# Performance work log

Hardware: AMD Instinct MI355X
Metric: run time of the kernel (lower is better)

The kernel has to match this reference:

```python
import jax, jax.numpy as jnp
import numpy as np
import math

N_HEADS = 16
D_MODEL = 1024
DK = D_MODEL // N_HEADS
B, S = 2, 2048


def setup_inputs() -> dict:
    key = jax.random.key(0)
    ks = jax.random.split(key, 11)
    scale_in = 1.0 / math.sqrt(D_MODEL)
    scale_o = 1.0 / math.sqrt(N_HEADS * DK)
    return {
        "query": jax.random.normal(ks[0], (B, S, D_MODEL), jnp.float32),
        "key": jax.random.normal(ks[1], (B, S, D_MODEL), jnp.float32),
        "value": jax.random.normal(ks[2], (B, S, D_MODEL), jnp.float32),
        # stacked per-head projection weights [H, d_model, dk], biases [H, dk]
        "Wq": jax.random.normal(ks[3], (N_HEADS, D_MODEL, DK), jnp.float32) * scale_in,
        "bq": jax.random.normal(ks[4], (N_HEADS, DK), jnp.float32) * scale_in,
        "Wk": jax.random.normal(ks[5], (N_HEADS, D_MODEL, DK), jnp.float32) * scale_in,
        "bk": jax.random.normal(ks[6], (N_HEADS, DK), jnp.float32) * scale_in,
        "Wv": jax.random.normal(ks[7], (N_HEADS, D_MODEL, DK), jnp.float32) * scale_in,
        "bv": jax.random.normal(ks[8], (N_HEADS, DK), jnp.float32) * scale_in,
        "Wo": jax.random.normal(ks[9], (N_HEADS * DK, D_MODEL), jnp.float32) * scale_o,
        "bo": jax.random.normal(ks[10], (D_MODEL,), jnp.float32) * scale_o,
    }


def reference(query, key, value, Wq, bq, Wk, bk, Wv, bv, Wo, bo):
    # Per-head linear projections, vectorized over heads: [B,H,S,dk]
    q = jnp.einsum("bsd,hdk->bhsk", query, Wq) + bq[None, :, None, :]
    k = jnp.einsum("bsd,hdk->bhsk", key, Wk) + bk[None, :, None, :]
    v = jnp.einsum("bsd,hdk->bhsk", value, Wv) + bv[None, :, None, :]
    # Scaled dot-product scores [B,H,S,S]
    scores = jnp.einsum("bhsk,bhtk->bhst", q, k) / jnp.sqrt(jnp.asarray(DK, q.dtype))
    # FAITHFUL to source: nn.Softmax(dim=0) -> softmax over the BATCH axis
    attn = jax.nn.softmax(scores, axis=0)
    out = jnp.einsum("bhst,bhtk->bhsk", attn, v)  # [B,H,S,dk]
    # concat heads along feature dim (torch.cat dim=2)
    concat = out.transpose(0, 2, 1, 3).reshape(query.shape[0], query.shape[1], N_HEADS * DK)
    return concat @ Wo + bo
```

## Files before the change

kernel.cpp:

```cpp
#include <hip/hip_runtime.h>
#include <hip/hip_bf16.h>

#define B_ 2
#define S_ 2048
#define D_ 1024
#define H_ 16
#define DK_ 64
#define BS_ (B_ * S_)

typedef unsigned int u32;
typedef unsigned short u16;
typedef __attribute__((ext_vector_type(8))) short bf16x8;
typedef __attribute__((ext_vector_type(4))) float f32x4;

__device__ __forceinline__ float bf2f(u16 v) {
    union { u32 u; float f; } c; c.u = ((u32)v) << 16; return c.f;
}
__device__ __forceinline__ u16 f2bf(float f) {
    union { float f; u32 u; } c; c.f = f;
    u32 u = c.u;
    return (u16)((u + 0x7fffu + ((u >> 16) & 1u)) >> 16);
}
__device__ __forceinline__ u32 packtr(float lo, float hi) {
    union { float f; u32 u; } a, b; a.f = lo; b.f = hi;
    return __builtin_amdgcn_perm(b.u, a.u, 0x07060302u);
}
__device__ __forceinline__ int sw64(int r, int c8) { return (((c8) + (r)) & 7) * 8; }
__device__ __forceinline__ int sw32(int r, int c8) { return (((c8) + (r)) & 3) * 8; }

struct WArgs { const float* W[4]; u16* WT[4]; };
__global__ __launch_bounds__(256) void prep_w(WArgs wa)
{
    __shared__ __attribute__((aligned(16))) u16 T[64][72];
    const int z = blockIdx.z;
    const float* W = wa.W[z];
    u16* WT = wa.WT[z];
    const int headMode = (z < 3) ? 1 : 0;
    const int tid = threadIdx.x;
    const int k0 = blockIdx.x * 64;
    const int n0 = blockIdx.y * 64;
    const int kr = tid >> 4;
    const int n4 = (tid & 15) * 4;
    #pragma unroll
    for (int pass = 0; pass < 4; ++pass) {
        int kk = k0 + pass * 16 + kr;
        const float* p = headMode
            ? (W + (size_t)((n0 + n4) >> 6) * (1024 * 64) + kk * 64 + ((n0 + n4) & 63))
            : (W + (size_t)kk * 1024 + n0 + n4);
        float4 a = *(const float4*)p;
        int krel = pass * 16 + kr;
        T[n4 + 0][krel] = f2bf(a.x);
        T[n4 + 1][krel] = f2bf(a.y);
        T[n4 + 2][krel] = f2bf(a.z);
        T[n4 + 3][krel] = f2bf(a.w);
    }
    __syncthreads();
    const int nr = tid >> 2;
    const int kq = (tid & 3) * 16;
    uint4 o0 = *(const uint4*)&T[nr][kq];
    uint4 o1 = *(const uint4*)&T[nr][kq + 8];
    u16* q = WT + (size_t)(n0 + nr) * 1024 + k0 + kq;
    *(uint4*)q = o0;
    *(uint4*)(q + 8) = o1;
}

__global__ __launch_bounds__(256) void vprep(
    const u16* __restrict__ Vb, u16* __restrict__ VT, float* __restrict__ csums)
{
    __shared__ __attribute__((aligned(16))) u16 T[64][72];
    __shared__ float red[256];
    const int tid = threadIdx.x;
    const int t0 = blockIdx.x * 64;
    const int bh = blockIdx.y;
    const int b = bh >> 4, h = bh & 15;
    const int tr = tid >> 4;
    const int d4 = (tid & 15) * 4;
    #pragma unroll
    for (int pass = 0; pass < 4; ++pass) {
        int tt = t0 + pass * 16 + tr;
        const u16* p = Vb + (size_t)(b * S_ + tt) * 1024 + h * 64 + d4;
        u32 a = *(const u32*)p;
        u32 c = *(const u32*)(p + 2);
        int trel = pass * 16 + tr;
        T[d4 + 0][trel] = (u16)a;
        T[d4 + 1][trel] = (u16)(a >> 16);
        T[d4 + 2][trel] = (u16)c;
        T[d4 + 3][trel] = (u16)(c >> 16);
    }
    __syncthreads();
    const int dr = tid >> 2;
    const int tq = (tid & 3) * 16;
    uint4 o0 = *(const uint4*)&T[dr][tq];
    uint4 o1 = *(const uint4*)&T[dr][tq + 8];
    u16* q = VT + ((size_t)bh * 64 + dr) * 2048 + t0 + tq;
    *(uint4*)q = o0;
    *(uint4*)(q + 8) = o1;

    if (b == 1) {
        const int dk = tid & 63, part = tid >> 6;
        float s = 0.f;
        #pragma unroll
        for (int t = 0; t < 16; ++t) s += bf2f(T[dk][part * 16 + t]);
        red[tid] = s;
        __syncthreads();
        if (tid < 64)
            atomicAdd(&csums[h * 64 + tid],
                      red[tid] + red[tid + 64] + red[tid + 128] + red[tid + 192]);
    }
}

struct ProjArgs {
    const float* X[3];
    const u16* W[3];
    const float* bias[3];
    u16* Y[3];
};
__global__ __launch_bounds__(256) void proj3(ProjArgs pa)
{
    __shared__ __attribute__((aligned(16))) u16 As[128][32];
    __shared__ __attribute__((aligned(16))) u16 Bs[64][32];
    const int z = blockIdx.z;
    const float* X = pa.X[z];
    const u16* WT = pa.W[z];
    const float* bias = pa.bias[z];
    u16* Y = pa.Y[z];
    const int neg = (z == 1);

    const int tid = threadIdx.x;
    const int lane = tid & 63;
    const int wave = tid >> 6;
    const int quad = lane >> 4;
    const int l16 = lane & 15;
    const int m0 = blockIdx.x * 128;
    const int n0 = blockIdx.y * 64;
    const int wm = (wave & 1) * 64, wn = (wave >> 1) * 32;

    const int srow = tid >> 1, half = tid & 1;
    const int brow = tid >> 2, bc8 = tid & 3;

    f32x4 acc[4][2] = {};

    for (int k0 = 0; k0 < 1024; k0 += 32) {
        __syncthreads();
        {
            const float* p = X + (size_t)(m0 + srow) * 1024 + k0 + half * 16;
            float4 a0 = *(const float4*)(p + 0);
            float4 a1 = *(const float4*)(p + 4);
            float4 a2 = *(const float4*)(p + 8);
            float4 a3 = *(const float4*)(p + 12);
            uint4 w0 = make_uint4(packtr(a0.x, a0.y), packtr(a0.z, a0.w),
                                  packtr(a1.x, a1.y), packtr(a1.z, a1.w));
            uint4 w1 = make_uint4(packtr(a2.x, a2.y), packtr(a2.z, a2.w),
                                  packtr(a3.x, a3.y), packtr(a3.z, a3.w));
            const int c8 = half * 2;
            *(uint4*)&As[srow][sw32(srow, c8)]     = w0;
            *(uint4*)&As[srow][sw32(srow, c8 + 1)] = w1;
            *(uint4*)&Bs[brow][sw32(brow, bc8)] =
                *(const uint4*)(WT + (size_t)(n0 + brow) * 1024 + k0 + bc8 * 8);
        }
        __syncthreads();
        bf16x8 af[4], bfr[2];
        #pragma unroll
        for (int mt = 0; mt < 4; ++mt) {
            const int r = wm + mt * 16 + l16;
            af[mt] = *(const bf16x8*)&As[r][sw32(r, quad)];
        }
        #pragma unroll
        for (int nt = 0; nt < 2; ++nt) {
            const int r = wn + nt * 16 + l16;
            bfr[nt] = *(const bf16x8*)&Bs[r][sw32(r, quad)];
        }
        #pragma unroll
        for (int mt = 0; mt < 4; ++mt)
            #pragma unroll
            for (int nt = 0; nt < 2; ++nt)
                acc[mt][nt] = __builtin_amdgcn_mfma_f32_16x16x32_bf16(
                    af[mt], bfr[nt], acc[mt][nt], 0, 0, 0);
    }

    #pragma unroll
    for (int nt = 0; nt < 2; ++nt) {
        const int col = n0 + wn + nt * 16 + l16;
        const float bv = bias[col];
        #pragma unroll
        for (int mt = 0; mt < 4; ++mt) {
            #pragma unroll
            for (int r = 0; r < 4; ++r) {
                const int row = m0 + wm + mt * 16 + quad * 4 + r;
                float v = acc[mt][nt][r] + bv;
                if (neg && row >= 2048) v = -v;
                Y[(size_t)row * 1024 + col] = f2bf(v);
            }
        }
    }
}

__global__ __launch_bounds__(256) void gemm_out(
    const u16* __restrict__ X, const u16* __restrict__ WT,
    const float* __restrict__ bias, float* __restrict__ Y)
{
    __shared__ __attribute__((aligned(16))) u16 As[128][32];
    __shared__ __attribute__((aligned(16))) u16 Bs[64][32];
    const int tid = threadIdx.x;
    const int lane = tid & 63;
    const int wave = tid >> 6;
    const int quad = lane >> 4;
    const int l16 = lane & 15;
    const int m0 = blockIdx.x * 128;
    const int n0 = blockIdx.y * 64;
    const int wm = (wave & 1) * 64, wn = (wave >> 1) * 32;

    const int srow = tid >> 1, half = tid & 1;
    const int brow = tid >> 2, bc8 = tid & 3;

    f32x4 acc[4][2] = {};

    for (int k0 = 0; k0 < 1024; k0 += 32) {
        __syncthreads();
        {
            const u16* p = X + (size_t)(m0 + srow) * 1024 + k0 + half * 16;
            const int c8 = half * 2;
            *(uint4*)&As[srow][sw32(srow, c8)]     = *(const uint4*)p;
            *(uint4*)&As[srow][sw32(srow, c8 + 1)] = *(const uint4*)(p + 8);
            *(uint4*)&Bs[brow][sw32(brow, bc8)] =
                *(const uint4*)(WT + (size_t)(n0 + brow) * 1024 + k0 + bc8 * 8);
        }
        __syncthreads();
        bf16x8 af[4], bfr[2];
        #pragma unroll
        for (int mt = 0; mt < 4; ++mt) {
            const int r = wm + mt * 16 + l16;
            af[mt] = *(const bf16x8*)&As[r][sw32(r, quad)];
        }
        #pragma unroll
        for (int nt = 0; nt < 2; ++nt) {
            const int r = wn + nt * 16 + l16;
            bfr[nt] = *(const bf16x8*)&Bs[r][sw32(r, quad)];
        }
        #pragma unroll
        for (int mt = 0; mt < 4; ++mt)
            #pragma unroll
            for (int nt = 0; nt < 2; ++nt)
                acc[mt][nt] = __builtin_amdgcn_mfma_f32_16x16x32_bf16(
                    af[mt], bfr[nt], acc[mt][nt], 0, 0, 0);
    }

    #pragma unroll
    for (int nt = 0; nt < 2; ++nt) {
        const int col = n0 + wn + nt * 16 + l16;
        const float bv = bias[col];
        #pragma unroll
        for (int mt = 0; mt < 4; ++mt) {
            #pragma unroll
            for (int r = 0; r < 4; ++r) {
                const int row = m0 + wm + mt * 16 + quad * 4 + r;
                Y[(size_t)row * 1024 + col] = acc[mt][nt][r] + bv;
            }
        }
    }
}

__global__ __launch_bounds__(256) void attn_mfma(
    const u16* __restrict__ Qb, const u16* __restrict__ Kb,
    const u16* __restrict__ VT, const float* __restrict__ csums,
    u16* __restrict__ Cc)
{
    __shared__ __attribute__((aligned(16))) u16 Ks[2][64][64];
    __shared__ __attribute__((aligned(16))) u16 Vs[2][64][64];
    __shared__ __attribute__((aligned(16))) u16 Ps[64][64];

    const int id = blockIdx.x;
    const int xcd = id & 7, j = id >> 3;
    const int h = xcd + 8 * (j >> 5);
    const int s0 = (j & 31) * 64;

    const int tid = threadIdx.x;
    const int lane = tid & 63;
    const int wave = tid >> 6;
    const int quad = lane >> 4;
    const int l16 = lane & 15;
    const int sw = wave * 16;

    const int r_ = tid >> 2;
    const int cq = (tid & 3) * 16;
    const int cq8 = (tid & 3) * 2;

    bf16x8 qf[2][2];
    #pragma unroll
    for (int b = 0; b < 2; ++b)
        #pragma unroll
        for (int ks = 0; ks < 2; ++ks)
            qf[b][ks] = *(const bf16x8*)(Qb + (size_t)(b * S_ + s0 + sw + l16) * 1024
                                          + h * 64 + ks * 32 + quad * 8);

    f32x4 O0[4] = {}, T1[4] = {};

    for (int t0 = 0; t0 < S_; t0 += 64) {
        __syncthreads();
        #pragma unroll
        for (int b = 0; b < 2; ++b) {
            const u16* pk = Kb + (size_t)(b * S_ + t0 + r_) * 1024 + h * 64 + cq;
            *(uint4*)&Ks[b][r_][sw64(r_, cq8)]     = *(const uint4*)pk;
            *(uint4*)&Ks[b][r_][sw64(r_, cq8 + 1)] = *(const uint4*)(pk + 8);
            const u16* pv = VT + ((size_t)(b * H_ + h) * 64 + r_) * 2048 + t0 + cq;
            *(uint4*)&Vs[b][r_][sw64(r_, cq8)]     = *(const uint4*)pv;
            *(uint4*)&Vs[b][r_][sw64(r_, cq8 + 1)] = *(const uint4*)(pv + 8);
        }
        __syncthreads();

        f32x4 dacc[4] = {};
        #pragma unroll
        for (int mt = 0; mt < 4; ++mt) {
            const int kr = mt * 16 + l16;
            #pragma unroll
            for (int ks = 0; ks < 2; ++ks) {
                bf16x8 k0f = *(const bf16x8*)&Ks[0][kr][sw64(kr, ks * 4 + quad)];
                dacc[mt] = __builtin_amdgcn_mfma_f32_16x16x32_bf16(k0f, qf[0][ks], dacc[mt], 0, 0, 0);
                bf16x8 k1f = *(const bf16x8*)&Ks[1][kr][sw64(kr, ks * 4 + quad)];
                dacc[mt] = __builtin_amdgcn_mfma_f32_16x16x32_bf16(k1f, qf[1][ks], dacc[mt], 0, 0, 0);
            }
        }
        const int pr = sw + l16;
        #pragma unroll
        for (int mt = 0; mt < 4; ++mt) {
            float p[4];
            #pragma unroll
            for (int r = 0; r < 4; ++r) {
                float e = __expf(dacc[mt][r] * -0.125f);
                p[r] = __builtin_amdgcn_rcpf(1.0f + e);
            }
            uint2 w;
            w.x = packtr(p[0], p[1]);
            w.y = packtr(p[2], p[3]);
            const int c8 = 2 * mt + (quad >> 1);
            *(uint2*)&Ps[pr][sw64(pr, c8) + (quad & 1) * 4] = w;
        }
        bf16x8 pf0 = *(const bf16x8*)&Ps[pr][sw64(pr, quad)];
        bf16x8 pf1 = *(const bf16x8*)&Ps[pr][sw64(pr, 4 + quad)];
        #pragma unroll
        for (int nt = 0; nt < 4; ++nt) {
            const int vr = nt * 16 + l16;
            bf16x8 v00 = *(const bf16x8*)&Vs[0][vr][sw64(vr, quad)];
            bf16x8 v01 = *(const bf16x8*)&Vs[0][vr][sw64(vr, 4 + quad)];
            O0[nt] = __builtin_amdgcn_mfma_f32_16x16x32_bf16(pf0, v00, O0[nt], 0, 0, 0);
            O0[nt] = __builtin_amdgcn_mfma_f32_16x16x32_bf16(pf1, v01, O0[nt], 0, 0, 0);
            bf16x8 v10 = *(const bf16x8*)&Vs[1][vr][sw64(vr, quad)];
            bf16x8 v11 = *(const bf16x8*)&Vs[1][vr][sw64(vr, 4 + quad)];
            T1[nt] = __builtin_amdgcn_mfma_f32_16x16x32_bf16(pf0, v10, T1[nt], 0, 0, 0);
            T1[nt] = __builtin_amdgcn_mfma_f32_16x16x32_bf16(pf1, v11, T1[nt], 0, 0, 0);
        }
    }

    #pragma unroll
    for (int nt = 0; nt < 4; ++nt) {
        const int dk = nt * 16 + l16;
        const float cs1 = csums[h * 64 + dk];
        #pragma unroll
        for (int r = 0; r < 4; ++r) {
            const int s = s0 + sw + quad * 4 + r;
            Cc[(size_t)(0 * S_ + s) * 1024 + h * 64 + dk] = f2bf(O0[nt][r]);
            Cc[(size_t)(1 * S_ + s) * 1024 + h * 64 + dk] = f2bf(cs1 - T1[nt][r]);
        }
    }
}

extern "C" void kernel_launch(void* const* d_in, const int* in_sizes, int n_in,
                              void* d_out, int out_size, void* d_ws, size_t ws_size,
                              hipStream_t stream) {
    const float* q  = (const float*)d_in[0];
    const float* k  = (const float*)d_in[1];
    const float* v  = (const float*)d_in[2];
    const float* Wq = (const float*)d_in[3];
    const float* bq = (const float*)d_in[4];
    const float* Wk = (const float*)d_in[5];
    const float* bk = (const float*)d_in[6];
    const float* Wv = (const float*)d_in[7];
    const float* bv = (const float*)d_in[8];
    const float* Wo = (const float*)d_in[9];
    const float* bo = (const float*)d_in[10];

    char* ws = (char*)d_ws;
    const size_t MB = 1024 * 1024;
    u16* Cc  = (u16*)(ws);
    u16* WqT = (u16*)(ws + 8  * MB);
    u16* WkT = (u16*)(ws + 10 * MB);
    u16* WvT = (u16*)(ws + 12 * MB);
    u16* WoT = (u16*)(ws + 14 * MB);
    u16* Qp  = (u16*)(ws + 16 * MB);
    u16* Kp  = (u16*)(ws + 24 * MB);
    u16* Vp  = (u16*)(ws + 32 * MB);
    u16* VTv = (u16*)(ws + 40 * MB);
    float* csums = (float*)d_out;

    dim3 blk(256);

    WArgs wa;
    wa.W[0] = Wq; wa.W[1] = Wk; wa.W[2] = Wv; wa.W[3] = Wo;
    wa.WT[0] = WqT; wa.WT[1] = WkT; wa.WT[2] = WvT; wa.WT[3] = WoT;
    prep_w<<<dim3(16, 16, 4), blk, 0, stream>>>(wa);

    ProjArgs pa;
    pa.X[0] = q;  pa.X[1] = k;  pa.X[2] = v;
    pa.W[0] = WqT; pa.W[1] = WkT; pa.W[2] = WvT;
    pa.bias[0] = bq; pa.bias[1] = bk; pa.bias[2] = bv;
    pa.Y[0] = Qp; pa.Y[1] = Kp; pa.Y[2] = Vp;
    proj3<<<dim3(32, 16, 3), blk, 0, stream>>>(pa);

    hipMemsetAsync(d_out, 0, 1024 * sizeof(float), stream);
    vprep<<<dim3(32, 32), blk, 0, stream>>>(Vp, VTv, csums);
    attn_mfma<<<dim3(512), blk, 0, stream>>>(Qp, Kp, VTv, csums, Cc);
    gemm_out<<<dim3(32, 16), blk, 0, stream>>>(Cc, WoT, bo, (float*)d_out);
}
```

Before: 276.5 us.

## Enlarge projection GEMM tiles, deepen K step, and fold csums memset into prep_w

The QKV projection kernel moves from 128x64 to 128x128 output tiles per block with a K step of 64, so each wave computes a 64x64 sub-tile and reuses its A and B fragments across more MFMAs. The output GEMM also moves to a K step of 64, halving barrier count. Both drop the XOR swizzle in favour of padded (72-wide) LDS rows to avoid bank conflicts. The separate memset of the column-sum buffer is removed and done by one prep_w block, saving a launch. The risks are higher register and LDS use, which lowers occupancy, and fewer blocks in the projection grid.

```diff
diff --git a/kernel.cpp b/kernel.cpp
--- a/kernel.cpp
+++ b/kernel.cpp
@@ -26,9 +26,8 @@
     return __builtin_amdgcn_perm(b.u, a.u, 0x07060302u);
 }
 __device__ __forceinline__ int sw64(int r, int c8) { return (((c8) + (r)) & 7) * 8; }
-__device__ __forceinline__ int sw32(int r, int c8) { return (((c8) + (r)) & 3) * 8; }
-
-struct WArgs { const float* W[4]; u16* WT[4]; };
+
+struct WArgs { const float* W[4]; u16* WT[4]; float* csums; };
 __global__ __launch_bounds__(256) void prep_w(WArgs wa)
 {
     __shared__ __attribute__((aligned(16))) u16 T[64][72];
@@ -37,6 +36,10 @@
     u16* WT = wa.WT[z];
     const int headMode = (z < 3) ? 1 : 0;
     const int tid = threadIdx.x;
+    if (z == 0 && blockIdx.x == 0 && blockIdx.y == 0) {
+        float4 zz = {0.f, 0.f, 0.f, 0.f};
+        *(float4*)(wa.csums + tid * 4) = zz;
+    }
     const int k0 = blockIdx.x * 64;
     const int n0 = blockIdx.y * 64;
     const int kr = tid >> 4;
@@ -117,8 +120,8 @@
 };
 __global__ __launch_bounds__(256) void proj3(ProjArgs pa)
 {
-    __shared__ __attribute__((aligned(16))) u16 As[128][32];
-    __shared__ __attribute__((aligned(16))) u16 Bs[64][32];
+    __shared__ __attribute__((aligned(16))) u16 As[128][72];
+    __shared__ __attribute__((aligned(16))) u16 Bs[128][72];
     const int z = blockIdx.z;
     const float* X = pa.X[z];
     const u16* WT = pa.W[z];
@@ -126,6 +129,84 @@
     u16* Y = pa.Y[z];
     const int neg = (z == 1);
 
+    const int tid = threadIdx.x;
+    const int lane = tid & 63;
+    const int wave = tid >> 6;
+    const int quad = lane >> 4;
+    const int l16 = lane & 15;
+    const int m0 = blockIdx.x * 128;
+    const int n0 = blockIdx.y * 128;
+    const int wm = (wave & 1) * 64, wn = (wave >> 1) * 64;
+
+    const int srow = tid >> 1;
+    const int scol = (tid & 1) * 32;
+
+    f32x4 acc[4][4] = {};
+
+    for (int k0 = 0; k0 < 1024; k0 += 64) {
+        __syncthreads();
+        {
+            const float* p = X + (size_t)(m0 + srow) * 1024 + k0 + scol;
+            #pragma unroll
+            for (int j = 0; j < 2; ++j) {
+                float4 a0 = *(const float4*)(p + j * 16 + 0);
+                float4 a1 = *(const float4*)(p + j * 16 + 4);
+                float4 a2 = *(const float4*)(p + j * 16 + 8);
+                float4 a3 = *(const float4*)(p + j * 16 + 12);
+                uint4 w0 = make_uint4(packtr(a0.x, a0.y), packtr(a0.z, a0.w),
+                                      packtr(a1.x, a1.y), packtr(a1.z, a1.w));
+                uint4 w1 = make_uint4(packtr(a2.x, a2.y), packtr(a2.z, a2.w),
+                                      packtr(a3.x, a3.y), packtr(a3.z, a3.w));
+                *(uint4*)&As[srow][scol + j * 16]     = w0;
+                *(uint4*)&As[srow][scol + j * 16 + 8] = w1;
+            }
+            const u16* q = WT + (size_t)(n0 + srow) * 1024 + k0 + scol;
+            #pragma unroll
+            for (int j = 0; j < 4; ++j)
+                *(uint4*)&Bs[srow][scol + j * 8] = *(const uint4*)(q + j * 8);
+        }
+        __syncthreads();
+        #pragma unroll
+        for (int ks = 0; ks < 2; ++ks) {
+            bf16x8 af[4], bfr[4];
+            #pragma unroll
+            for (int mt = 0; mt < 4; ++mt)
+                af[mt] = *(const bf16x8*)&As[wm + mt * 16 + l16][ks * 32 + quad * 8];
+            #pragma unroll
+            for (int nt = 0; nt < 4; ++nt)
+                bfr[nt] = *(const bf16x8*)&Bs[wn + nt * 16 + l16][ks * 32 + quad * 8];
+            #pragma unroll
+            for (int mt = 0; mt < 4; ++mt)
+                #pragma unroll
+                for (int nt = 0; nt < 4; ++nt)
+                    acc[mt][nt] = __builtin_amdgcn_mfma_f32_16x16x32_bf16(
+                        af[mt], bfr[nt], acc[mt][nt], 0, 0, 0);
+        }
+    }
+
+    #pragma unroll
+    for (int nt = 0; nt < 4; ++nt) {
+        const int col = n0 + wn + nt * 16 + l16;
+        const float bv = bias[col];
+        #pragma unroll
+        for (int mt = 0; mt < 4; ++mt) {
+            #pragma unroll
+            for (int r = 0; r < 4; ++r) {
+                const int row = m0 + wm + mt * 16 + quad * 4 + r;
+                float v = acc[mt][nt][r] + bv;
+                if (neg && row >= 2048) v = -v;
+                Y[(size_t)row * 1024 + col] = f2bf(v);
+            }
+        }
+    }
+}
+
+__global__ __launch_bounds__(256) void gemm_out(
+    const u16* __restrict__ X, const u16* __restrict__ WT,
+    const float* __restrict__ bias, float* __restrict__ Y)
+{
+    __shared__ __attribute__((aligned(16))) u16 As[128][72];
+    __shared__ __attribute__((aligned(16))) u16 Bs[64][72];
     const int tid = threadIdx.x;
     const int lane = tid & 63;
     const int wave = tid >> 6;
@@ -135,114 +216,41 @@
     const int n0 = blockIdx.y * 64;
     const int wm = (wave & 1) * 64, wn = (wave >> 1) * 32;
 
-    const int srow = tid >> 1, half = tid & 1;
-    const int brow = tid >> 2, bc8 = tid & 3;
+    const int srow = tid >> 1;
+    const int scol = (tid & 1) * 32;
+    const int brow = tid >> 2;
+    const int bcol = (tid & 3) * 16;
 
     f32x4 acc[4][2] = {};
 
-    for (int k0 = 0; k0 < 1024; k0 += 32) {
+    for (int k0 = 0; k0 < 1024; k0 += 64) {
         __syncthreads();
         {
-            const float* p = X + (size_t)(m0 + srow) * 1024 + k0 + half * 16;
-            float4 a0 = *(const float4*)(p + 0);
-            float4 a1 = *(const float4*)(p + 4);
-            float4 a2 = *(const float4*)(p + 8);
-            float4 a3 = *(const float4*)(p + 12);
-            uint4 w0 = make_uint4(packtr(a0.x, a0.y), packtr(a0.z, a0.w),
-                                  packtr(a1.x, a1.y), packtr(a1.z, a1.w));
-            uint4 w1 = make_uint4(packtr(a2.x, a2.y), packtr(a2.z, a2.w),
-                                  packtr(a3.x, a3.y), packtr(a3.z, a3.w));
-            const int c8 = half * 2;
-            *(uint4*)&As[srow][sw32(srow, c8)]     = w0;
-            *(uint4*)&As[srow][sw32(srow, c8 + 1)] = w1;
-            *(uint4*)&Bs[brow][sw32(brow, bc8)] =
-                *(const uint4*)(WT + (size_t)(n0 + brow) * 1024 + k0 + bc8 * 8);
-        }
-        __syncthreads();
-        bf16x8 af[4], bfr[2];
-        #pragma unroll
-        for (int mt = 0; mt < 4; ++mt) {
-            const int r = wm + mt * 16 + l16;
-            af[mt] = *(const bf16x8*)&As[r][sw32(r, quad)];
-        }
-        #pragma unroll
-        for (int nt = 0; nt < 2; ++nt) {
-            const int r = wn + nt * 16 + l16;
-            bfr[nt] = *(const bf16x8*)&Bs[r][sw32(r, quad)];
-        }
-        #pragma unroll
-        for (int mt = 0; mt < 4; ++mt)
+            const u16* p = X + (size_t)(m0 + srow) * 1024 + k0 + scol;
+            #pragma unroll
+            for (int j = 0; j < 4; ++j)
+                *(uint4*)&As[srow][scol + j * 8] = *(const uint4*)(p + j * 8);
+            const u16* q = WT + (size_t)(n0 + brow) * 1024 + k0 + bcol;
+            *(uint4*)&Bs[brow][bcol]     = *(const uint4*)q;
+            *(uint4*)&Bs[brow][bcol + 8] = *(const uint4*)(q + 8);
+        }
+        __syncthreads();
+        #pragma unroll
+        for (int ks = 0; ks < 2; ++ks) {
+            bf16x8 af[4], bfr[2];
+            #pragma unroll
+            for (int mt = 0; mt < 4; ++mt)
+                af[mt] = *(const bf16x8*)&As[wm + mt * 16 + l16][ks * 32 + quad * 8];
             #pragma unroll
             for (int nt = 0; nt < 2; ++nt)
-                acc[mt][nt] = __builtin_amdgcn_mfma_f32_16x16x32_bf16(
-                    af[mt], bfr[nt], acc[mt][nt], 0, 0, 0);
-    }
-
-    #pragma unroll
-    for (int nt = 0; nt < 2; ++nt) {
-        const int col = n0 + wn + nt * 16 + l16;
-        const float bv = bias[col];
-        #pragma unroll
-        for (int mt = 0; mt < 4; ++mt) {
-            #pragma unroll
-            for (int r = 0; r < 4; ++r) {
-                const int row = m0 + wm + mt * 16 + quad * 4 + r;
-                float v = acc[mt][nt][r] + bv;
-                if (neg && row >= 2048) v = -v;
-                Y[(size_t)row * 1024 + col] = f2bf(v);
-            }
-        }
-    }
-}
-
-__global__ __launch_bounds__(256) void gemm_out(
-    const u16* __restrict__ X, const u16* __restrict__ WT,
-    const float* __restrict__ bias, float* __restrict__ Y)
-{
-    __shared__ __attribute__((aligned(16))) u16 As[128][32];
-    __shared__ __attribute__((aligned(16))) u16 Bs[64][32];
-    const int tid = threadIdx.x;
-    const int lane = tid & 63;
-    const int wave = tid >> 6;
-    const int quad = lane >> 4;
-    const int l16 = lane & 15;
-    const int m0 = blockIdx.x * 128;
-    const int n0 = blockIdx.y * 64;
-    const int wm = (wave & 1) * 64, wn = (wave >> 1) * 32;
-
-    const int srow = tid >> 1, half = tid & 1;
-    const int brow = tid >> 2, bc8 = tid & 3;
-
-    f32x4 acc[4][2] = {};
-
-    for (int k0 = 0; k0 < 1024; k0 += 32) {
-        __syncthreads();
-        {
-            const u16* p = X + (size_t)(m0 + srow) * 1024 + k0 + half * 16;
-            const int c8 = half * 2;
-            *(uint4*)&As[srow][sw32(srow, c8)]     = *(const uint4*)p;
-            *(uint4*)&As[srow][sw32(srow, c8 + 1)] = *(const uint4*)(p + 8);
-            *(uint4*)&Bs[brow][sw32(brow, bc8)] =
-                *(const uint4*)(WT + (size_t)(n0 + brow) * 1024 + k0 + bc8 * 8);
-        }
-        __syncthreads();
-        bf16x8 af[4], bfr[2];
-        #pragma unroll
-        for (int mt = 0; mt < 4; ++mt) {
-            const int r = wm + mt * 16 + l16;
-            af[mt] = *(const bf16x8*)&As[r][sw32(r, quad)];
-        }
-        #pragma unroll
-        for (int nt = 0; nt < 2; ++nt) {
-            const int r = wn + nt * 16 + l16;
-            bfr[nt] = *(const bf16x8*)&Bs[r][sw32(r, quad)];
-        }
-        #pragma unroll
-        for (int mt = 0; mt < 4; ++mt)
-            #pragma unroll
-            for (int nt = 0; nt < 2; ++nt)
-                acc[mt][nt] = __builtin_amdgcn_mfma_f32_16x16x32_bf16(
-                    af[mt], bfr[nt], acc[mt][nt], 0, 0, 0);
+                bfr[nt] = *(const bf16x8*)&Bs[wn + nt * 16 + l16][ks * 32 + quad * 8];
+            #pragma unroll
+            for (int mt = 0; mt < 4; ++mt)
+                #pragma unroll
+                for (int nt = 0; nt < 2; ++nt)
+                    acc[mt][nt] = __builtin_amdgcn_mfma_f32_16x16x32_bf16(
+                        af[mt], bfr[nt], acc[mt][nt], 0, 0, 0);
+        }
     }
 
     #pragma unroll
@@ -397,6 +405,7 @@
     WArgs wa;
     wa.W[0] = Wq; wa.W[1] = Wk; wa.W[2] = Wv; wa.W[3] = Wo;
     wa.WT[0] = WqT; wa.WT[1] = WkT; wa.WT[2] = WvT; wa.WT[3] = WoT;
+    wa.csums = csums;
     prep_w<<<dim3(16, 16, 4), blk, 0, stream>>>(wa);
 
     ProjArgs pa;
@@ -404,9 +413,8 @@
     pa.W[0] = WqT; pa.W[1] = WkT; pa.W[2] = WvT;
     pa.bias[0] = bq; pa.bias[1] = bk; pa.bias[2] = bv;
     pa.Y[0] = Qp; pa.Y[1] = Kp; pa.Y[2] = Vp;
-    proj3<<<dim3(32, 16, 3), blk, 0, stream>>>(pa);
-
-    hipMemsetAsync(d_out, 0, 1024 * sizeof(float), stream);
+    proj3<<<dim3(32, 8, 3), blk, 0, stream>>>(pa);
+
     vprep<<<dim3(32, 32), blk, 0, stream>>>(Vp, VTv, csums);
     attn_mfma<<<dim3(512), blk, 0, stream>>>(Qp, Kp, VTv, csums, Cc);
     gemm_out<<<dim3(32, 16), blk, 0, stream>>>(Cc, WoT, bo, (float*)d_out);
```

New measurement: 259.2 us. -6.3%, faster.
